# Optimization experiments

Measured on AMD Instinct MI355X. Metric: run time of the kernel, lower is better.

The kernel has to match this reference:

```python
import jax, jax.numpy as jnp
import numpy as np

D_MODEL = 384
D_INNER = 768
D_STATE = 16
DT_RANK = 24
D_CONV = 4
N_BLOCKS = 6
EPS = 1e-5


def setup_inputs() -> dict:
    key = jax.random.key(0)
    ks = jax.random.split(key, 16)
    s = 0.05
    x = jax.random.normal(ks[0], (1, 8, 16, 16, D_MODEL), jnp.float32)
    inp = {
        'x': x,
        'norm_w': jnp.ones((N_BLOCKS, D_MODEL), jnp.float32),
        'in_proj_w': s * jax.random.normal(ks[1], (N_BLOCKS, 2 * D_INNER, D_MODEL), jnp.float32),
        'conv_w': s * jax.random.normal(ks[2], (N_BLOCKS, D_INNER, D_CONV), jnp.float32),
        'conv_b': jnp.zeros((N_BLOCKS, D_INNER), jnp.float32),
        'x_proj_w': s * jax.random.normal(ks[3], (N_BLOCKS, DT_RANK + 2 * D_STATE, D_INNER), jnp.float32),
        'dt_proj_w': s * jax.random.normal(ks[4], (N_BLOCKS, D_INNER, DT_RANK), jnp.float32),
        'dt_proj_b': jnp.full((N_BLOCKS, D_INNER), -2.0, jnp.float32),  # softplus(-2) ~ small init dt
        'A_log': jnp.broadcast_to(jnp.log(jnp.arange(1, D_STATE + 1, dtype=jnp.float32)), (N_BLOCKS, D_INNER, D_STATE)).copy(),
        'D_param': jnp.ones((N_BLOCKS, D_INNER), jnp.float32),
        'out_proj_w': s * jax.random.normal(ks[5], (N_BLOCKS, D_MODEL, D_INNER), jnp.float32),
    }
    return inp


def _rmsnorm(x, w):
    var = jnp.mean(x * x, axis=-1, keepdims=True)
    return x * jax.lax.rsqrt(var + EPS) * w


def _causal_conv1d(x, w, b):
    # x: (N, L, C), w: (C, k) depthwise, causal left-pad
    xt = jnp.transpose(x, (0, 2, 1))  # (N, C, L)
    out = jax.lax.conv_general_dilated(
        xt, w[:, None, :], window_strides=(1,), padding=[(w.shape[-1] - 1, 0)],
        dimension_numbers=('NCH', 'OIH', 'NCH'), feature_group_count=w.shape[0])
    return jnp.transpose(out, (0, 2, 1)) + b


def _selective_scan(u, delta, A, Bm, Cm, Dp):
    # u, delta: (N, L, d_in); A: (d_in, d_state); Bm, Cm: (N, L, d_state)
    dA = jnp.exp(delta[..., None] * A)                      # (N, L, d_in, d_state)
    dBu = delta[..., None] * Bm[:, :, None, :] * u[..., None]

    def step(h, inp):
        dA_t, dBu_t, C_t = inp
        h = dA_t * h + dBu_t                                # (N, d_in, d_state)
        y = jnp.einsum('nds,ns->nd', h, C_t)
        return h, y

    h0 = jnp.zeros((u.shape[0], u.shape[2], A.shape[1]), u.dtype)
    _, ys = jax.lax.scan(step, h0, (jnp.transpose(dA, (1, 0, 2, 3)),
                                    jnp.transpose(dBu, (1, 0, 2, 3)),
                                    jnp.transpose(Cm, (1, 0, 2))))
    y = jnp.transpose(ys, (1, 0, 2))                        # (N, L, d_in)
    return y + u * Dp


def _mamba_layer(x, p):
    # pre-norm residual Mamba mixer; x: (N, L, D_MODEL)
    h = _rmsnorm(x, p['norm_w'])
    xz = jnp.einsum('nld,ed->nle', h, p['in_proj_w'])       # (N, L, 2*d_inner)
    xp, z = jnp.split(xz, 2, axis=-1)
    xp = jax.nn.silu(_causal_conv1d(xp, p['conv_w'], p['conv_b']))
    x_dbl = jnp.einsum('nld,ed->nle', xp, p['x_proj_w'])
    dt, Bm, Cm = jnp.split(x_dbl, [DT_RANK, DT_RANK + D_STATE], axis=-1)
    dt = jax.nn.softplus(jnp.einsum('nlr,dr->nld', dt, p['dt_proj_w']) + p['dt_proj_b'])
    A = -jnp.exp(p['A_log'])
    y = _selective_scan(xp, dt, A, Bm, Cm, p['D_param'])
    y = y * jax.nn.silu(z)
    return x + jnp.einsum('nle,de->nld', y, p['out_proj_w'])


def _block(x, params, i):
    p = {k: v[i] for k, v in params.items()}
    return _mamba_layer(x, p)


def reference(x, norm_w, in_proj_w, conv_w, conv_b, x_proj_w, dt_proj_w, dt_proj_b, A_log, D_param, out_proj_w):
    params = dict(norm_w=norm_w, in_proj_w=in_proj_w, conv_w=conv_w, conv_b=conv_b,
                  x_proj_w=x_proj_w, dt_proj_w=dt_proj_w, dt_proj_b=dt_proj_b,
                  A_log=A_log, D_param=D_param, out_proj_w=out_proj_w)
    N, L, H, W, D = x.shape
    # HWL ordering
    h = jnp.transpose(x, (0, 2, 3, 1, 4)).reshape(N, H * W * L, D)
    h = _block(h, params, 0)                                 # hwl
    h = _block(h[:, ::-1], params, 1)[:, ::-1]               # r_hwl
    # LWH ordering
    h = h.reshape(N, H, W, L, D)
    h = jnp.transpose(h, (0, 3, 2, 1, 4)).reshape(N, L * W * H, D)
    h = _block(h, params, 2)                                 # lwh
    h = _block(h[:, ::-1], params, 3)[:, ::-1]               # r_lwh
    # LHW ordering
    h = h.reshape(N, L, W, H, D)
    h = jnp.transpose(h, (0, 1, 3, 2, 4)).reshape(N, L * H * W, D)
    h = _block(h, params, 4)                                 # lhw
    h = _block(h[:, ::-1], params, 5)[:, ::-1]               # r_lhw
    return h.reshape(N, L, H, W, D)
```

## Files before the change

### kernel.cpp

```cpp
#include <hip/hip_runtime.h>
#include <math.h>

#define D_MODEL 384
#define D_INNER 768
#define D_STATE 16
#define DT_RANK 24
#define NTOK    2048
#define XDIM    56
#define CHUNK   32
#define NCHUNK  (NTOK / CHUNK)

typedef __attribute__((ext_vector_type(8))) short bf16x8;
typedef __attribute__((ext_vector_type(4))) float f32x4;

__device__ __forceinline__ int tok_of(int order, int p) {
    int q = (order & 1) ? (NTOK - 1 - p) : p;
    int grp = order >> 1;
    int l, h, w;
    if (grp == 0)      { h = q >> 7;  w = (q >> 3) & 15; l = q & 7;  }
    else if (grp == 1) { l = q >> 8;  w = (q >> 4) & 15; h = q & 15; }
    else               { return q; }
    return l * 256 + h * 16 + w;
}

__device__ __forceinline__ float sigmoidf_(float x) { return 1.f / (1.f + expf(-x)); }
__device__ __forceinline__ float softplusf_(float x) { return (x > 20.f) ? x : log1pf(expf(x)); }

__device__ __forceinline__ void bf16split_(float a, unsigned short& hb, unsigned short& lb) {
    unsigned int ab = __float_as_uint(a);
    hb = (unsigned short)(ab >> 16);
    float hf = __uint_as_float(ab & 0xFFFF0000u);
    lb = (unsigned short)(__float_as_uint(a - hf) >> 16);
}

__global__ __launch_bounds__(256) void presplit_k(
    const float* __restrict__ A, unsigned short* __restrict__ H,
    unsigned short* __restrict__ L, int n4)
{
    const int i = blockIdx.x * 256 + threadIdx.x;
    if (i >= n4) return;
    const float4 v = ((const float4*)A)[i];
    ushort4 h, l;
    bf16split_(v.x, h.x, l.x);
    bf16split_(v.y, h.y, l.y);
    bf16split_(v.z, h.z, l.z);
    bf16split_(v.w, h.w, l.w);
    ((ushort4*)H)[i] = h;
    ((ushort4*)L)[i] = l;
}

__global__ __launch_bounds__(128) void rmsnorm_gather_k(
    const float* __restrict__ R, const float* __restrict__ nw,
    unsigned short* __restrict__ Xnh, unsigned short* __restrict__ Xnl, int order)
{
    const int p   = blockIdx.x;
    const int tok = tok_of(order, p);
    const float* src = R + tok * D_MODEL;
    const int tid = threadIdx.x;
    float v0 = src[tid], v1 = src[tid + 128], v2 = src[tid + 256];
    float ss = v0 * v0 + v1 * v1 + v2 * v2;
#pragma unroll
    for (int off = 32; off > 0; off >>= 1) ss += __shfl_xor(ss, off);
    __shared__ float tot[2];
    if ((tid & 63) == 0) tot[tid >> 6] = ss;
    __syncthreads();
    const float rs = rsqrtf((tot[0] + tot[1]) * (1.f / D_MODEL) + 1e-5f);
    unsigned short h, l;
    bf16split_(v0 * rs * nw[tid], h, l);
    Xnh[p * D_MODEL + tid] = h;       Xnl[p * D_MODEL + tid] = l;
    bf16split_(v1 * rs * nw[tid + 128], h, l);
    Xnh[p * D_MODEL + tid + 128] = h; Xnl[p * D_MODEL + tid + 128] = l;
    bf16split_(v2 * rs * nw[tid + 256], h, l);
    Xnh[p * D_MODEL + tid + 256] = h; Xnl[p * D_MODEL + tid + 256] = l;
}

__global__ __launch_bounds__(256, 3) void inproj_mfma_k(
    const unsigned short* __restrict__ Ahg, const unsigned short* __restrict__ Alg,
    const unsigned short* __restrict__ WH, const unsigned short* __restrict__ WL,
    float* __restrict__ XP, float* __restrict__ GT)
{
    __shared__ __align__(16) short Ah[4 * 64 * 8];
    __shared__ __align__(16) short Al[4 * 64 * 8];
    __shared__ __align__(16) short Bh[4 * 64 * 8];
    __shared__ __align__(16) short Bl[4 * 64 * 8];

    const int tid = threadIdx.x;
    const int m0 = blockIdx.y * 64;
    const int n0 = blockIdx.x * 64;
    const int w  = tid >> 6;
    const int l  = tid & 63;
    const int lr = l & 15;
    const int kg = l >> 4;
    const int srow = tid >> 2;
    const int skq  = tid & 3;

    f32x4 acc[4];
#pragma unroll
    for (int r = 0; r < 4; ++r) acc[r] = (f32x4){0.f, 0.f, 0.f, 0.f};

    for (int k0 = 0; k0 < D_MODEL; k0 += 32) {
        const int aoff = (m0 + srow) * D_MODEL + k0 + skq * 8;
        const int woff = (n0 + srow) * D_MODEL + k0 + skq * 8;
        const int soff = (skq * 64 + srow) * 8;
        *(bf16x8*)&Ah[soff] = *(const bf16x8*)&Ahg[aoff];
        *(bf16x8*)&Al[soff] = *(const bf16x8*)&Alg[aoff];
        *(bf16x8*)&Bh[soff] = *(const bf16x8*)&WH[woff];
        *(bf16x8*)&Bl[soff] = *(const bf16x8*)&WL[woff];
        __syncthreads();

        const bf16x8 bh = *(const bf16x8*)&Bh[(kg * 64 + w * 16 + lr) * 8];
        const bf16x8 bl = *(const bf16x8*)&Bl[(kg * 64 + w * 16 + lr) * 8];
#pragma unroll
        for (int r = 0; r < 4; ++r) {
            const bf16x8 ah = *(const bf16x8*)&Ah[(kg * 64 + r * 16 + lr) * 8];
            const bf16x8 al = *(const bf16x8*)&Al[(kg * 64 + r * 16 + lr) * 8];
            acc[r] = __builtin_amdgcn_mfma_f32_16x16x32_bf16(ah, bh, acc[r], 0, 0, 0);
            acc[r] = __builtin_amdgcn_mfma_f32_16x16x32_bf16(ah, bl, acc[r], 0, 0, 0);
            acc[r] = __builtin_amdgcn_mfma_f32_16x16x32_bf16(al, bh, acc[r], 0, 0, 0);
        }
        __syncthreads();
    }

    const int n = n0 + w * 16 + lr;
    if (n0 < D_INNER) {
#pragma unroll
        for (int r = 0; r < 4; ++r)
#pragma unroll
            for (int i = 0; i < 4; ++i) {
                const int t = m0 + r * 16 + kg * 4 + i;
                XP[t * D_INNER + n] = acc[r][i];
            }
    } else {
        const int n2 = n - D_INNER;
#pragma unroll
        for (int r = 0; r < 4; ++r)
#pragma unroll
            for (int i = 0; i < 4; ++i) {
                const int t = m0 + r * 16 + kg * 4 + i;
                const float c = acc[r][i];
                GT[n2 * NTOK + t] = c * sigmoidf_(c);
            }
    }
}

__global__ __launch_bounds__(256, 3) void outproj_mfma_k(
    const float* __restrict__ YG, const unsigned short* __restrict__ WH,
    const unsigned short* __restrict__ WL, float* __restrict__ PO)
{
    __shared__ __align__(16) short Ah[4 * 64 * 8];
    __shared__ __align__(16) short Al[4 * 64 * 8];
    __shared__ __align__(16) short Bh[4 * 64 * 8];
    __shared__ __align__(16) short Bl[4 * 64 * 8];

    const int tid = threadIdx.x;
    const int m0 = blockIdx.y * 64;
    const int n0 = blockIdx.x * 64;
    const int kb = blockIdx.z * 384;
    const int w  = tid >> 6;
    const int l  = tid & 63;
    const int lr = l & 15;
    const int kg = l >> 4;
    const int srow = tid >> 2;
    const int skq  = tid & 3;

    f32x4 acc[4];
#pragma unroll
    for (int r = 0; r < 4; ++r) acc[r] = (f32x4){0.f, 0.f, 0.f, 0.f};

    for (int k0 = 0; k0 < 384; k0 += 32) {
        const float* ap = YG + (m0 + srow) * D_INNER + kb + k0 + skq * 8;
        const float4 a0 = *(const float4*)ap;
        const float4 a1 = *(const float4*)(ap + 4);
        const float av[8] = {a0.x, a0.y, a0.z, a0.w, a1.x, a1.y, a1.z, a1.w};
        union { bf16x8 v; unsigned short u[8]; } hu, lu;
#pragma unroll
        for (int j = 0; j < 8; ++j) bf16split_(av[j], hu.u[j], lu.u[j]);
        const int soff = (skq * 64 + srow) * 8;
        *(bf16x8*)&Ah[soff] = hu.v;
        *(bf16x8*)&Al[soff] = lu.v;
        const int woff = (n0 + srow) * D_INNER + kb + k0 + skq * 8;
        *(bf16x8*)&Bh[soff] = *(const bf16x8*)&WH[woff];
        *(bf16x8*)&Bl[soff] = *(const bf16x8*)&WL[woff];
        __syncthreads();

        const bf16x8 bh = *(const bf16x8*)&Bh[(kg * 64 + w * 16 + lr) * 8];
        const bf16x8 bl = *(const bf16x8*)&Bl[(kg * 64 + w * 16 + lr) * 8];
#pragma unroll
        for (int r = 0; r < 4; ++r) {
            const bf16x8 ah = *(const bf16x8*)&Ah[(kg * 64 + r * 16 + lr) * 8];
            const bf16x8 al = *(const bf16x8*)&Al[(kg * 64 + r * 16 + lr) * 8];
            acc[r] = __builtin_amdgcn_mfma_f32_16x16x32_bf16(ah, bh, acc[r], 0, 0, 0);
            acc[r] = __builtin_amdgcn_mfma_f32_16x16x32_bf16(ah, bl, acc[r], 0, 0, 0);
            acc[r] = __builtin_amdgcn_mfma_f32_16x16x32_bf16(al, bh, acc[r], 0, 0, 0);
        }
        __syncthreads();
    }

    float* Cz = PO + (size_t)blockIdx.z * NTOK * D_MODEL;
    const int n = n0 + w * 16 + lr;
#pragma unroll
    for (int r = 0; r < 4; ++r)
#pragma unroll
        for (int i = 0; i < 4; ++i) {
            const int t = m0 + r * 16 + kg * 4 + i;
            Cz[t * D_MODEL + n] = acc[r][i];
        }
}

template<int MODE, bool TRANSA>
__global__ __launch_bounds__(256, 2) void gemm_k(
    const float* __restrict__ A, int lda,
    const float* __restrict__ W,
    float* __restrict__ C,
    int M, int N, int K,
    const float* __restrict__ bias,
    float* __restrict__ C2,
    int kspan)
{
    __shared__ float As[16][68];
    __shared__ float Ws[16][68];
    const int tid = threadIdx.x;
    const int m0 = blockIdx.y * 64;
    const int n0 = blockIdx.x * 64;
    const int tx = tid & 15, ty = tid >> 4;
    const int lrow = tid >> 2;
    const int lk   = (tid & 3) << 2;
    const int kb   = blockIdx.z * kspan;
    const int ke   = (kb + kspan < K) ? (kb + kspan) : K;
    float acc[4][4] = {{0.f}};

    for (int k0 = kb; k0 < ke; k0 += 16) {
        if (TRANSA) {
            const int kk = k0 + (tid & 15);
            const int mq = tid >> 4;
            float4 v = make_float4(0.f, 0.f, 0.f, 0.f);
            if (kk < K) v = *(const float4*)&A[kk * lda + m0 + mq * 4];
            *(float4*)&As[tid & 15][mq * 4] = v;
        } else {
            const int m = m0 + lrow;
            const float* src = A + m * lda + (k0 + lk);
            float4 v = make_float4(0.f, 0.f, 0.f, 0.f);
            if (k0 + lk + 3 < K) v = *(const float4*)src;
            else {
                if (k0 + lk + 0 < K) v.x = src[0];
                if (k0 + lk + 1 < K) v.y = src[1];
                if (k0 + lk + 2 < K) v.z = src[2];
            }
            As[lk + 0][lrow] = v.x; As[lk + 1][lrow] = v.y;
            As[lk + 2][lrow] = v.z; As[lk + 3][lrow] = v.w;
        }
        {
            const int n = n0 + lrow;
            float4 u = make_float4(0.f, 0.f, 0.f, 0.f);
            if (n < N) {
                const float* srcw = W + n * K + (k0 + lk);
                if (k0 + lk + 3 < K) u = *(const float4*)srcw;
                else {
                    if (k0 + lk + 0 < K) u.x = srcw[0];
                    if (k0 + lk + 1 < K) u.y = srcw[1];
                    if (k0 + lk + 2 < K) u.z = srcw[2];
                }
            }
            Ws[lk + 0][lrow] = u.x; Ws[lk + 1][lrow] = u.y;
            Ws[lk + 2][lrow] = u.z; Ws[lk + 3][lrow] = u.w;
        }
        __syncthreads();
#pragma unroll
        for (int k = 0; k < 16; ++k) {
            float4 a4 = *(const float4*)&As[k][ty * 4];
            float4 w4 = *(const float4*)&Ws[k][tx * 4];
            float ar[4] = {a4.x, a4.y, a4.z, a4.w};
            float wr[4] = {w4.x, w4.y, w4.z, w4.w};
#pragma unroll
            for (int i = 0; i < 4; ++i)
#pragma unroll
                for (int j = 0; j < 4; ++j)
                    acc[i][j] = fmaf(ar[i], wr[j], acc[i][j]);
        }
        __syncthreads();
    }

    const int row0 = m0 + ty * 4;
    const int col0 = n0 + tx * 4;
    if (MODE == 3) {
        float* Cz = C + (size_t)blockIdx.z * N * NTOK;
#pragma unroll
        for (int j = 0; j < 4; ++j) {
            const int col = col0 + j;
            if (col < N) {
                float4 v = make_float4(acc[0][j], acc[1][j], acc[2][j], acc[3][j]);
                *(float4*)&Cz[col * NTOK + row0] = v;
            }
        }
    } else if (MODE == 4) {
#pragma unroll
        for (int j = 0; j < 4; ++j) {
            const int col = col0 + j;
            if (col < N) {
                const float bv = bias[col];
                float4 v = make_float4(softplusf_(acc[0][j] + bv), softplusf_(acc[1][j] + bv),
                                       softplusf_(acc[2][j] + bv), softplusf_(acc[3][j] + bv));
                *(float4*)&C[col * NTOK + row0] = v;
            }
        }
    }
}

__global__ __launch_bounds__(256) void reduce_px_k(
    const float* __restrict__ PX, float* __restrict__ XDT)
{
    const int i4 = blockIdx.x * 256 + threadIdx.x;
    float4 s = ((const float4*)PX)[i4];
#pragma unroll
    for (int z = 1; z < 8; ++z) {
        float4 v = ((const float4*)PX)[z * (XDIM * NTOK / 4) + i4];
        s.x += v.x; s.y += v.y; s.z += v.z; s.w += v.w;
    }
    ((float4*)XDT)[i4] = s;
}

__global__ __launch_bounds__(384) void reduce_scatter_k(
    const float* __restrict__ PO, float* __restrict__ R, int order)
{
    const int m = blockIdx.x;
    const int col = threadIdx.x;
    float s = PO[m * D_MODEL + col] + PO[NTOK * D_MODEL + m * D_MODEL + col];
    const int tok = tok_of(order, m);
    R[tok * D_MODEL + col] += s;
}

__global__ __launch_bounds__(256) void conv_silu_t_k(
    const float* __restrict__ XP, const float* __restrict__ cw,
    const float* __restrict__ cb, float* __restrict__ XCT)
{
    __shared__ float xs[67][33];
    const int c0 = blockIdx.x * 32;
    const int t0 = blockIdx.y * 64;
    const int tid = threadIdx.x;
    const int col = tid & 31, rr = tid >> 5;
#pragma unroll
    for (int r = rr; r < 67; r += 8) {
        const int t = t0 - 3 + r;
        xs[r][col] = (t >= 0) ? XP[t * D_INNER + c0 + col] : 0.f;
    }
    __syncthreads();
    const int tl = tid & 63;
#pragma unroll
    for (int cl = tid >> 6; cl < 32; cl += 4) {
        const int c = c0 + cl;
        const float4 w4 = *(const float4*)(cw + c * 4);
        float acc = cb[c];
        acc = fmaf(w4.x, xs[tl + 0][cl], acc);
        acc = fmaf(w4.y, xs[tl + 1][cl], acc);
        acc = fmaf(w4.z, xs[tl + 2][cl], acc);
        acc = fmaf(w4.w, xs[tl + 3][cl], acc);
        XCT[c * NTOK + t0 + tl] = acc * sigmoidf_(acc);
    }
}

__global__ __launch_bounds__(256) void scan_phase1_k(
    const float* __restrict__ XCT, const float* __restrict__ DTT,
    const float* __restrict__ XDT, const float* __restrict__ A_log,
    float* __restrict__ Aprod, float* __restrict__ Hpart)
{
    const int tid = threadIdx.x;
    const int s = tid & 15;
    const int d = blockIdx.x * 16 + (tid >> 4);
    const int chunk = blockIdx.y;
    const float Aneg = -expf(A_log[d * D_STATE + s]);
    const float* dtp = DTT + d * NTOK + chunk * CHUNK;
    const float* up  = XCT + d * NTOK + chunk * CHUNK;
    const float* Bp  = XDT + (DT_RANK + s) * NTOK + chunk * CHUNK;
    float h = 0.f, ap = 1.f;
#pragma unroll
    for (int tt = 0; tt < CHUNK; tt += 4) {
        const float4 dt4 = *(const float4*)(dtp + tt);
        const float4 u4  = *(const float4*)(up + tt);
        const float4 B4  = *(const float4*)(Bp + tt);
        float a;
        a = expf(dt4.x * Aneg); h = fmaf(a, h, dt4.x * B4.x * u4.x); ap *= a;
        a = expf(dt4.y * Aneg); h = fmaf(a, h, dt4.y * B4.y * u4.y); ap *= a;
        a = expf(dt4.z * Aneg); h = fmaf(a, h, dt4.z * B4.z * u4.z); ap *= a;
        a = expf(dt4.w * Aneg); h = fmaf(a, h, dt4.w * B4.w * u4.w); ap *= a;
    }
    const int idx = (chunk * D_INNER + d) * D_STATE + s;
    Aprod[idx] = ap;
    Hpart[idx] = h;
}

__global__ __launch_bounds__(256) void scan_phase2_k(
    const float* __restrict__ Aprod, const float* __restrict__ Hpart,
    float* __restrict__ Hinit)
{
    const int tid = blockIdx.x * 256 + threadIdx.x;
    float h = 0.f;
#pragma unroll 8
    for (int c = 0; c < NCHUNK; ++c) {
        const int idx = c * (D_INNER * D_STATE) + tid;
        Hinit[idx] = h;
        h = fmaf(Aprod[idx], h, Hpart[idx]);
    }
}

__global__ __launch_bounds__(256) void scan_phase3_k(
    const float* __restrict__ XCT, const float* __restrict__ DTT,
    const float* __restrict__ XDT, const float* __restrict__ GT,
    const float* __restrict__ A_log, const float* __restrict__ Dp,
    const float* __restrict__ Hinit, float* __restrict__ YG)
{
    const int tid = threadIdx.x;
    const int s = tid & 15;
    const int d = blockIdx.x * 16 + (tid >> 4);
    const int chunk = blockIdx.y;
    const float Aneg = -expf(A_log[d * D_STATE + s]);
    const float Dv = Dp[d];
    const float* dtp = DTT + d * NTOK + chunk * CHUNK;
    const float* up  = XCT + d * NTOK + chunk * CHUNK;
    const float* Bp  = XDT + (DT_RANK + s) * NTOK + chunk * CHUNK;
    const float* Cp  = XDT + (DT_RANK + D_STATE + s) * NTOK + chunk * CHUNK;
    const float* Gp  = GT  + d * NTOK + chunk * CHUNK;
    float h = Hinit[(chunk * D_INNER + d) * D_STATE + s];
#pragma unroll
    for (int tt = 0; tt < CHUNK; tt += 4) {
        const float4 dt4 = *(const float4*)(dtp + tt);
        const float4 u4  = *(const float4*)(up + tt);
        const float4 B4  = *(const float4*)(Bp + tt);
        const float4 C4  = *(const float4*)(Cp + tt);
        float a, p0, p1, p2, p3;
        a = expf(dt4.x * Aneg); h = fmaf(a, h, dt4.x * B4.x * u4.x); p0 = h * C4.x;
        a = expf(dt4.y * Aneg); h = fmaf(a, h, dt4.y * B4.y * u4.y); p1 = h * C4.y;
        a = expf(dt4.z * Aneg); h = fmaf(a, h, dt4.z * B4.z * u4.z); p2 = h * C4.z;
        a = expf(dt4.w * Aneg); h = fmaf(a, h, dt4.w * B4.w * u4.w); p3 = h * C4.w;
#pragma unroll
        for (int m = 1; m <= 8; m <<= 1) {
            p0 += __shfl_xor(p0, m); p1 += __shfl_xor(p1, m);
            p2 += __shfl_xor(p2, m); p3 += __shfl_xor(p3, m);
        }
        if (s == 0) {
            const float4 g4 = *(const float4*)(Gp + tt);
            const int tbase = chunk * CHUNK + tt;
            YG[(tbase + 0) * D_INNER + d] = (p0 + u4.x * Dv) * g4.x;
            YG[(tbase + 1) * D_INNER + d] = (p1 + u4.y * Dv) * g4.y;
            YG[(tbase + 2) * D_INNER + d] = (p2 + u4.z * Dv) * g4.z;
            YG[(tbase + 3) * D_INNER + d] = (p3 + u4.w * Dv) * g4.w;
        }
    }
}

extern "C" void kernel_launch(void* const* d_in, const int* in_sizes, int n_in,
                              void* d_out, int out_size, void* d_ws, size_t ws_size,
                              hipStream_t stream)
{
    const float* x        = (const float*)d_in[0];
    const float* norm_w   = (const float*)d_in[1];
    const float* in_proj  = (const float*)d_in[2];
    const float* conv_w   = (const float*)d_in[3];
    const float* conv_b   = (const float*)d_in[4];
    const float* x_proj   = (const float*)d_in[5];
    const float* dt_proj  = (const float*)d_in[6];
    const float* dt_b     = (const float*)d_in[7];
    const float* A_log    = (const float*)d_in[8];
    const float* D_param  = (const float*)d_in[9];
    const float* out_proj = (const float*)d_in[10];

    float* ws = (float*)d_ws;
    float* R     = ws;
    float* XP    = R   + 786432;
    float* XnHL  = XP  + 1572864;
    float* GT    = XnHL + 786432;
    float* XCT   = GT  + 1572864;
    float* XDT   = XCT + 1572864;
    float* DTT   = XDT + 114688;
    float* YG    = DTT + 1572864;
    float* WS1   = YG  + 1572864;
    unsigned short* Xnh  = (unsigned short*)XnHL;
    unsigned short* Xnl  = Xnh + 786432;
    unsigned short* WinH = (unsigned short*)WS1;
    unsigned short* WinL = WinH + 6 * 1536 * 384;
    unsigned short* WoutH = WinL + 6 * 1536 * 384;
    unsigned short* WoutL = WoutH + 6 * 384 * 768;
    float* Aprod = XnHL;
    float* Hpart = YG;
    float* Hinit = XP;
    float* PX    = XP;
    float* PO    = GT;

    hipMemcpyAsync(R, x, (size_t)786432 * sizeof(float), hipMemcpyDeviceToDevice, stream);

    presplit_k<<<(6 * 1536 * 384 / 4 + 255) / 256, 256, 0, stream>>>(
        in_proj, WinH, WinL, 6 * 1536 * 384 / 4);
    presplit_k<<<(6 * 384 * 768 / 4 + 255) / 256, 256, 0, stream>>>(
        out_proj, WoutH, WoutL, 6 * 384 * 768 / 4);

    for (int b = 0; b < 6; ++b) {
        rmsnorm_gather_k<<<NTOK, 128, 0, stream>>>(R, norm_w + b * D_MODEL, Xnh, Xnl, b);

        inproj_mfma_k<<<dim3(24, 32), 256, 0, stream>>>(
            Xnh, Xnl, WinH + (size_t)b * 1536 * 384, WinL + (size_t)b * 1536 * 384, XP, GT);

        conv_silu_t_k<<<dim3(24, 32), 256, 0, stream>>>(
            XP, conv_w + b * D_INNER * 4, conv_b + b * D_INNER, XCT);

        gemm_k<3, true><<<dim3(1, 32, 8), 256, 0, stream>>>(
            XCT, NTOK, x_proj + (size_t)b * XDIM * D_INNER, PX,
            NTOK, XDIM, D_INNER, nullptr, nullptr, 96);

        reduce_px_k<<<112, 256, 0, stream>>>(PX, XDT);

        gemm_k<4, true><<<dim3(12, 32, 1), 256, 0, stream>>>(
            XDT, NTOK, dt_proj + (size_t)b * D_INNER * DT_RANK, DTT,
            NTOK, D_INNER, DT_RANK, dt_b + b * D_INNER, nullptr, DT_RANK);

        scan_phase1_k<<<dim3(48, NCHUNK), 256, 0, stream>>>(
            XCT, DTT, XDT, A_log + (size_t)b * D_INNER * D_STATE, Aprod, Hpart);

        scan_phase2_k<<<48, 256, 0, stream>>>(Aprod, Hpart, Hinit);

        scan_phase3_k<<<dim3(48, NCHUNK), 256, 0, stream>>>(
            XCT, DTT, XDT, GT, A_log + (size_t)b * D_INNER * D_STATE,
            D_param + b * D_INNER, Hinit, YG);

        outproj_mfma_k<<<dim3(6, 32, 2), 256, 0, stream>>>(
            YG, WoutH + (size_t)b * 384 * 768, WoutL + (size_t)b * 384 * 768, PO);

        reduce_scatter_k<<<NTOK, 384, 0, stream>>>(PO, R, b);
    }

    hipMemcpyAsync(d_out, R, (size_t)786432 * sizeof(float), hipMemcpyDeviceToDevice, stream);
}
```

Before: 900.8 us.

## Switch intermediates to token-major layout and scan all states per thread

Stores the gate, conv output and delta buffers token-major instead of channel-major. The conv becomes a simple per-element kernel, x_proj reads its input non-transposed, and dt_proj writes row-major with the softplus bias. The scan kernels now give each thread one channel and all 16 states in registers, with B and C staged in shared memory, which removes the cross-lane shuffle reduction. In exchange the scan grid shrinks from 48x64 to 3x64 blocks, lowering parallelism and raising register pressure.

```diff
diff --git a/kernel.cpp b/kernel.cpp
--- a/kernel.cpp
+++ b/kernel.cpp
@@ -77,7 +77,7 @@
 __global__ __launch_bounds__(256, 3) void inproj_mfma_k(
     const unsigned short* __restrict__ Ahg, const unsigned short* __restrict__ Alg,
     const unsigned short* __restrict__ WH, const unsigned short* __restrict__ WL,
-    float* __restrict__ XP, float* __restrict__ GT)
+    float* __restrict__ XP, float* __restrict__ G)
 {
     __shared__ __align__(16) short Ah[4 * 64 * 8];
     __shared__ __align__(16) short Al[4 * 64 * 8];
@@ -138,7 +138,7 @@
             for (int i = 0; i < 4; ++i) {
                 const int t = m0 + r * 16 + kg * 4 + i;
                 const float c = acc[r][i];
-                GT[n2 * NTOK + t] = c * sigmoidf_(c);
+                G[t * D_INNER + n2] = c * sigmoidf_(c);
             }
     }
 }
@@ -282,7 +282,15 @@
 
     const int row0 = m0 + ty * 4;
     const int col0 = n0 + tx * 4;
-    if (MODE == 3) {
+    if (MODE == 1) {
+        const float4 bv = *(const float4*)&bias[col0];
+#pragma unroll
+        for (int i = 0; i < 4; ++i) {
+            float4 v = make_float4(softplusf_(acc[i][0] + bv.x), softplusf_(acc[i][1] + bv.y),
+                                   softplusf_(acc[i][2] + bv.z), softplusf_(acc[i][3] + bv.w));
+            *(float4*)&C[(row0 + i) * N + col0] = v;
+        }
+    } else if (MODE == 3) {
         float* Cz = C + (size_t)blockIdx.z * N * NTOK;
 #pragma unroll
         for (int j = 0; j < 4; ++j) {
@@ -292,17 +300,6 @@
                 *(float4*)&Cz[col * NTOK + row0] = v;
             }
         }
-    } else if (MODE == 4) {
-#pragma unroll
-        for (int j = 0; j < 4; ++j) {
-            const int col = col0 + j;
-            if (col < N) {
-                const float bv = bias[col];
-                float4 v = make_float4(softplusf_(acc[0][j] + bv), softplusf_(acc[1][j] + bv),
-                                       softplusf_(acc[2][j] + bv), softplusf_(acc[3][j] + bv));
-                *(float4*)&C[col * NTOK + row0] = v;
-            }
-        }
     }
 }
 
@@ -329,63 +326,57 @@
     R[tok * D_MODEL + col] += s;
 }
 
-__global__ __launch_bounds__(256) void conv_silu_t_k(
+__global__ __launch_bounds__(256) void conv_silu_k(
     const float* __restrict__ XP, const float* __restrict__ cw,
-    const float* __restrict__ cb, float* __restrict__ XCT)
-{
-    __shared__ float xs[67][33];
-    const int c0 = blockIdx.x * 32;
-    const int t0 = blockIdx.y * 64;
-    const int tid = threadIdx.x;
-    const int col = tid & 31, rr = tid >> 5;
-#pragma unroll
-    for (int r = rr; r < 67; r += 8) {
-        const int t = t0 - 3 + r;
-        xs[r][col] = (t >= 0) ? XP[t * D_INNER + c0 + col] : 0.f;
-    }
-    __syncthreads();
-    const int tl = tid & 63;
-#pragma unroll
-    for (int cl = tid >> 6; cl < 32; cl += 4) {
-        const int c = c0 + cl;
-        const float4 w4 = *(const float4*)(cw + c * 4);
-        float acc = cb[c];
-        acc = fmaf(w4.x, xs[tl + 0][cl], acc);
-        acc = fmaf(w4.y, xs[tl + 1][cl], acc);
-        acc = fmaf(w4.z, xs[tl + 2][cl], acc);
-        acc = fmaf(w4.w, xs[tl + 3][cl], acc);
-        XCT[c * NTOK + t0 + tl] = acc * sigmoidf_(acc);
-    }
+    const float* __restrict__ cb, float* __restrict__ XC)
+{
+    const int d = blockIdx.x * 256 + threadIdx.x;
+    const int t = blockIdx.y;
+    const float4 w4 = *(const float4*)(cw + d * 4);
+    float acc = cb[d];
+    if (t >= 3) acc = fmaf(w4.x, XP[(t - 3) * D_INNER + d], acc);
+    if (t >= 2) acc = fmaf(w4.y, XP[(t - 2) * D_INNER + d], acc);
+    if (t >= 1) acc = fmaf(w4.z, XP[(t - 1) * D_INNER + d], acc);
+    acc = fmaf(w4.w, XP[t * D_INNER + d], acc);
+    XC[t * D_INNER + d] = acc * sigmoidf_(acc);
 }
 
 __global__ __launch_bounds__(256) void scan_phase1_k(
-    const float* __restrict__ XCT, const float* __restrict__ DTT,
+    const float* __restrict__ XC, const float* __restrict__ DT,
     const float* __restrict__ XDT, const float* __restrict__ A_log,
     float* __restrict__ Aprod, float* __restrict__ Hpart)
 {
-    const int tid = threadIdx.x;
-    const int s = tid & 15;
-    const int d = blockIdx.x * 16 + (tid >> 4);
+    __shared__ float Bs[CHUNK][D_STATE];
+    const int d = blockIdx.x * 256 + threadIdx.x;
     const int chunk = blockIdx.y;
-    const float Aneg = -expf(A_log[d * D_STATE + s]);
-    const float* dtp = DTT + d * NTOK + chunk * CHUNK;
-    const float* up  = XCT + d * NTOK + chunk * CHUNK;
-    const float* Bp  = XDT + (DT_RANK + s) * NTOK + chunk * CHUNK;
-    float h = 0.f, ap = 1.f;
-#pragma unroll
-    for (int tt = 0; tt < CHUNK; tt += 4) {
-        const float4 dt4 = *(const float4*)(dtp + tt);
-        const float4 u4  = *(const float4*)(up + tt);
-        const float4 B4  = *(const float4*)(Bp + tt);
-        float a;
-        a = expf(dt4.x * Aneg); h = fmaf(a, h, dt4.x * B4.x * u4.x); ap *= a;
-        a = expf(dt4.y * Aneg); h = fmaf(a, h, dt4.y * B4.y * u4.y); ap *= a;
-        a = expf(dt4.z * Aneg); h = fmaf(a, h, dt4.z * B4.z * u4.z); ap *= a;
-        a = expf(dt4.w * Aneg); h = fmaf(a, h, dt4.w * B4.w * u4.w); ap *= a;
-    }
-    const int idx = (chunk * D_INNER + d) * D_STATE + s;
-    Aprod[idx] = ap;
-    Hpart[idx] = h;
+    const int t0 = chunk * CHUNK;
+    for (int i = threadIdx.x; i < CHUNK * D_STATE; i += 256) {
+        const int tt = i >> 4, s = i & 15;
+        Bs[tt][s] = XDT[(DT_RANK + s) * NTOK + t0 + tt];
+    }
+    __syncthreads();
+    float An[D_STATE], h[D_STATE], ap[D_STATE];
+#pragma unroll
+    for (int s = 0; s < D_STATE; ++s) {
+        An[s] = -expf(A_log[d * D_STATE + s]);
+        h[s] = 0.f; ap[s] = 1.f;
+    }
+#pragma unroll 4
+    for (int tt = 0; tt < CHUNK; ++tt) {
+        const float dt = DT[(t0 + tt) * D_INNER + d];
+        const float u  = XC[(t0 + tt) * D_INNER + d];
+        const float dtu = dt * u;
+#pragma unroll
+        for (int s = 0; s < D_STATE; ++s) {
+            const float a = expf(dt * An[s]);
+            h[s] = fmaf(a, h[s], dtu * Bs[tt][s]);
+            ap[s] *= a;
+        }
+    }
+    float* apd = Aprod + (chunk * D_INNER + d) * D_STATE;
+    float* hpd = Hpart + (chunk * D_INNER + d) * D_STATE;
+#pragma unroll
+    for (int s = 0; s < D_STATE; ++s) { apd[s] = ap[s]; hpd[s] = h[s]; }
 }
 
 __global__ __launch_bounds__(256) void scan_phase2_k(
@@ -403,47 +394,44 @@
 }
 
 __global__ __launch_bounds__(256) void scan_phase3_k(
-    const float* __restrict__ XCT, const float* __restrict__ DTT,
-    const float* __restrict__ XDT, const float* __restrict__ GT,
+    const float* __restrict__ XC, const float* __restrict__ DT,
+    const float* __restrict__ XDT, const float* __restrict__ G,
     const float* __restrict__ A_log, const float* __restrict__ Dp,
     const float* __restrict__ Hinit, float* __restrict__ YG)
 {
-    const int tid = threadIdx.x;
-    const int s = tid & 15;
-    const int d = blockIdx.x * 16 + (tid >> 4);
+    __shared__ float Bs[CHUNK][D_STATE];
+    __shared__ float Cs[CHUNK][D_STATE];
+    const int d = blockIdx.x * 256 + threadIdx.x;
     const int chunk = blockIdx.y;
-    const float Aneg = -expf(A_log[d * D_STATE + s]);
+    const int t0 = chunk * CHUNK;
+    for (int i = threadIdx.x; i < CHUNK * D_STATE; i += 256) {
+        const int tt = i >> 4, s = i & 15;
+        Bs[tt][s] = XDT[(DT_RANK + s) * NTOK + t0 + tt];
+        Cs[tt][s] = XDT[(DT_RANK + D_STATE + s) * NTOK + t0 + tt];
+    }
+    __syncthreads();
     const float Dv = Dp[d];
-    const float* dtp = DTT + d * NTOK + chunk * CHUNK;
-    const float* up  = XCT + d * NTOK + chunk * CHUNK;
-    const float* Bp  = XDT + (DT_RANK + s) * NTOK + chunk * CHUNK;
-    const float* Cp  = XDT + (DT_RANK + D_STATE + s) * NTOK + chunk * CHUNK;
-    const float* Gp  = GT  + d * NTOK + chunk * CHUNK;
-    float h = Hinit[(chunk * D_INNER + d) * D_STATE + s];
-#pragma unroll
-    for (int tt = 0; tt < CHUNK; tt += 4) {
-        const float4 dt4 = *(const float4*)(dtp + tt);
-        const float4 u4  = *(const float4*)(up + tt);
-        const float4 B4  = *(const float4*)(Bp + tt);
-        const float4 C4  = *(const float4*)(Cp + tt);
-        float a, p0, p1, p2, p3;
-        a = expf(dt4.x * Aneg); h = fmaf(a, h, dt4.x * B4.x * u4.x); p0 = h * C4.x;
-        a = expf(dt4.y * Aneg); h = fmaf(a, h, dt4.y * B4.y * u4.y); p1 = h * C4.y;
-        a = expf(dt4.z * Aneg); h = fmaf(a, h, dt4.z * B4.z * u4.z); p2 = h * C4.z;
-        a = expf(dt4.w * Aneg); h = fmaf(a, h, dt4.w * B4.w * u4.w); p3 = h * C4.w;
-#pragma unroll
-        for (int m = 1; m <= 8; m <<= 1) {
-            p0 += __shfl_xor(p0, m); p1 += __shfl_xor(p1, m);
-            p2 += __shfl_xor(p2, m); p3 += __shfl_xor(p3, m);
-        }
-        if (s == 0) {
-            const float4 g4 = *(const float4*)(Gp + tt);
-            const int tbase = chunk * CHUNK + tt;
-            YG[(tbase + 0) * D_INNER + d] = (p0 + u4.x * Dv) * g4.x;
-            YG[(tbase + 1) * D_INNER + d] = (p1 + u4.y * Dv) * g4.y;
-            YG[(tbase + 2) * D_INNER + d] = (p2 + u4.z * Dv) * g4.z;
-            YG[(tbase + 3) * D_INNER + d] = (p3 + u4.w * Dv) * g4.w;
-        }
+    float An[D_STATE], h[D_STATE];
+    const float* hin = Hinit + (chunk * D_INNER + d) * D_STATE;
+#pragma unroll
+    for (int s = 0; s < D_STATE; ++s) {
+        An[s] = -expf(A_log[d * D_STATE + s]);
+        h[s] = hin[s];
+    }
+#pragma unroll 4
+    for (int tt = 0; tt < CHUNK; ++tt) {
+        const float dt = DT[(t0 + tt) * D_INNER + d];
+        const float u  = XC[(t0 + tt) * D_INNER + d];
+        const float g  = G[(t0 + tt) * D_INNER + d];
+        const float dtu = dt * u;
+        float y = 0.f;
+#pragma unroll
+        for (int s = 0; s < D_STATE; ++s) {
+            const float a = expf(dt * An[s]);
+            h[s] = fmaf(a, h[s], dtu * Bs[tt][s]);
+            y = fmaf(h[s], Cs[tt][s], y);
+        }
+        YG[(t0 + tt) * D_INNER + d] = (y + u * Dv) * g;
     }
 }
 
@@ -467,11 +455,11 @@
     float* R     = ws;
     float* XP    = R   + 786432;
     float* XnHL  = XP  + 1572864;
-    float* GT    = XnHL + 786432;
-    float* XCT   = GT  + 1572864;
-    float* XDT   = XCT + 1572864;
-    float* DTT   = XDT + 114688;
-    float* YG    = DTT + 1572864;
+    float* G     = XnHL + 786432;
+    float* XC    = G   + 1572864;
+    float* XDT   = XC  + 1572864;
+    float* DT    = XDT + 114688;
+    float* YG    = DT  + 1572864;
     float* WS1   = YG  + 1572864;
     unsigned short* Xnh  = (unsigned short*)XnHL;
     unsigned short* Xnl  = Xnh + 786432;
@@ -483,7 +471,7 @@
     float* Hpart = YG;
     float* Hinit = XP;
     float* PX    = XP;
-    float* PO    = GT;
+    float* PO    = G;
 
     hipMemcpyAsync(R, x, (size_t)786432 * sizeof(float), hipMemcpyDeviceToDevice, stream);
 
@@ -496,28 +484,28 @@
         rmsnorm_gather_k<<<NTOK, 128, 0, stream>>>(R, norm_w + b * D_MODEL, Xnh, Xnl, b);
 
         inproj_mfma_k<<<dim3(24, 32), 256, 0, stream>>>(
-            Xnh, Xnl, WinH + (size_t)b * 1536 * 384, WinL + (size_t)b * 1536 * 384, XP, GT);
-
-        conv_silu_t_k<<<dim3(24, 32), 256, 0, stream>>>(
-            XP, conv_w + b * D_INNER * 4, conv_b + b * D_INNER, XCT);
-
-        gemm_k<3, true><<<dim3(1, 32, 8), 256, 0, stream>>>(
-            XCT, NTOK, x_proj + (size_t)b * XDIM * D_INNER, PX,
+            Xnh, Xnl, WinH + (size_t)b * 1536 * 384, WinL + (size_t)b * 1536 * 384, XP, G);
+
+        conv_silu_k<<<dim3(3, NTOK), 256, 0, stream>>>(
+            XP, conv_w + b * D_INNER * 4, conv_b + b * D_INNER, XC);
+
+        gemm_k<3, false><<<dim3(1, 32, 8), 256, 0, stream>>>(
+            XC, D_INNER, x_proj + (size_t)b * XDIM * D_INNER, PX,
             NTOK, XDIM, D_INNER, nullptr, nullptr, 96);
 
         reduce_px_k<<<112, 256, 0, stream>>>(PX, XDT);
 
-        gemm_k<4, true><<<dim3(12, 32, 1), 256, 0, stream>>>(
-            XDT, NTOK, dt_proj + (size_t)b * D_INNER * DT_RANK, DTT,
+        gemm_k<1, true><<<dim3(12, 32, 1), 256, 0, stream>>>(
+            XDT, NTOK, dt_proj + (size_t)b * D_INNER * DT_RANK, DT,
             NTOK, D_INNER, DT_RANK, dt_b + b * D_INNER, nullptr, DT_RANK);
 
-        scan_phase1_k<<<dim3(48, NCHUNK), 256, 0, stream>>>(
-            XCT, DTT, XDT, A_log + (size_t)b * D_INNER * D_STATE, Aprod, Hpart);
+        scan_phase1_k<<<dim3(3, NCHUNK), 256, 0, stream>>>(
+            XC, DT, XDT, A_log + (size_t)b * D_INNER * D_STATE, Aprod, Hpart);
 
         scan_phase2_k<<<48, 256, 0, stream>>>(Aprod, Hpart, Hinit);
 
-        scan_phase3_k<<<dim3(48, NCHUNK), 256, 0, stream>>>(
-            XCT, DTT, XDT, GT, A_log + (size_t)b * D_INNER * D_STATE,
+        scan_phase3_k<<<dim3(3, NCHUNK), 256, 0, stream>>>(
+            XC, DT, XDT, G, A_log + (size_t)b * D_INNER * D_STATE,
             D_param + b * D_INNER, Hinit, YG);
 
         outproj_mfma_k<<<dim3(6, 32, 2), 256, 0, stream>>>(
```

Result: slower. 981.1 us (+8.9%).
